# Performance work log

Measured on AMD Instinct MI355X. Metric: run time of the kernel, lower is better.

## Reference

```python
import jax, jax.numpy as jnp
import numpy as np

B, S, D = 128, 1024, 256
K = 512  # num_clusters


def setup_inputs() -> dict:
    key = jax.random.key(0)
    k1, = jax.random.split(key, 1)
    inputs = jax.random.normal(k1, (B, S, D), dtype=jnp.float32)
    # init centroids as the first K data points so no cluster is empty
    centroids = inputs.reshape(-1, D)[:K]
    return {"inputs": inputs, "centroids": centroids}


def reference(inputs, centroids):
    d = inputs.shape[-1]
    k = centroids.shape[0]
    x = inputs.reshape(-1, d)                      # [N, D]
    # squared euclidean distances via GEMM decomposition (avoids N x K x D tensor)
    x2 = jnp.sum(x * x, axis=1, keepdims=True)     # [N, 1]
    c2 = jnp.sum(centroids * centroids, axis=1)    # [K]
    dist = x2 - 2.0 * (x @ centroids.T) + c2       # [N, K]
    idx = jnp.argmin(dist, axis=-1)                # [N]
    clusters = jax.nn.one_hot(idx, k, dtype=x.dtype)   # [N, K]
    counts = jnp.sum(clusters, axis=0)             # [K]
    sums = jnp.einsum('nk,nd->kd', clusters, x)    # [K, D] scatter-reduce as GEMM
    new_centroids = sums / counts[:, None]         # [K, D]
    updated_centroids = 0.9 * centroids + 0.1 * new_centroids  # EMA update
    clusters_out = clusters.reshape(inputs.shape[:-1] + (k,))  # [B, S, K]
    return clusters_out, updated_centroids
```

## Files before the change

### kernel.cpp

```cpp
#include <hip/hip_runtime.h>
#include <hip/hip_fp16.h>

#define NPTS 131072
#define DIM  256
#define KTOT 512
#define GAP_T 0.0625f

typedef unsigned short u16;
typedef _Float16 half8 __attribute__((ext_vector_type(8)));
typedef float floatx4 __attribute__((ext_vector_type(4)));

#define WS_MAIN_NEED 8394816u

__global__ __launch_bounds__(64)
void c2_kernel(const float* __restrict__ c, double* __restrict__ c2) {
  int k = blockIdx.x;
  int lane = threadIdx.x;
  const float* row = c + (size_t)k * DIM;
  double s = 0.0;
#pragma unroll
  for (int r = 0; r < DIM / 64; ++r) {
    float v = row[r * 64 + lane];
    s += (double)v * (double)v;
  }
#pragma unroll
  for (int off = 32; off > 0; off >>= 1) s += __shfl_down(s, off);
  if (lane == 0) c2[k] = s;
}

__global__ __launch_bounds__(256)
void csplit_kernel(const float* __restrict__ c, u16* __restrict__ Ch, u16* __restrict__ Cl) {
  int id = blockIdx.x * 256 + threadIdx.x;
  int n = id >> 5;
  int cg = id & 31;
  int kc = cg >> 3, cc = cg & 7;
  const float* src = c + (size_t)n * DIM + cg * 8;
  half8 hv, lv;
#pragma unroll
  for (int e = 0; e < 8; ++e) {
    float f = src[e];
    _Float16 h = (_Float16)f;
    hv[e] = h;
    lv[e] = (_Float16)(f - (float)h);
  }
  size_t dst = (size_t)n * DIM + kc * 64 + (size_t)(cc ^ (n & 7)) * 8;
  *(half8*)(Ch + dst) = hv;
  *(half8*)(Cl + dst) = lv;
}

__device__ __forceinline__ void load_lds16(const void* g, void* l) {
  __builtin_amdgcn_global_load_lds((const __attribute__((address_space(1))) void*)g,
                                   (__attribute__((address_space(3))) void*)l, 16, 0, 0);
}

__global__ __launch_bounds__(256)
void gemm_topk_kernel(const float* __restrict__ x, const u16* __restrict__ Ch,
                      const u16* __restrict__ Cl, const double* __restrict__ c2,
                      float* __restrict__ pv1, int* __restrict__ pk1, float* __restrict__ pv2) {
  __shared__ __align__(16) unsigned char smem[128 * 132 * 4];
  __shared__ float rb_v[128], rb_v2[128];
  __shared__ int rb_k[128];
  u16* Ah = (u16*)smem;
  u16* Al = Ah + 8192;
  u16* Bh = Al + 8192;
  u16* Bl = Bh + 8192;

  const int tid = threadIdx.x;
  const int bx = blockIdx.x;
  const int nblk = bx & 3, mblk = bx >> 2;
  const int m0 = mblk * 128, n0 = nblk * 128;
  const int w = tid >> 6, lane = tid & 63;
  const int wm = (w & 1) * 64, wn = (w >> 1) * 64;
  const int lm = lane & 15, quad = lane >> 4;

  floatx4 acc[4][4] = {};

  for (int kc = 0; kc < 4; ++kc) {
    const int k0 = kc * 64;
    __syncthreads();
#pragma unroll
    for (int i = 0; i < 4; ++i) {
      int s = i * 256 + tid;
      int row = s >> 3, pos = s & 7;
      size_t go = (size_t)(n0 + row) * DIM + k0 + pos * 8;
      load_lds16(Ch + go, Bh + (size_t)s * 8);
      load_lds16(Cl + go, Bl + (size_t)s * 8);
    }
#pragma unroll
    for (int i = 0; i < 4; ++i) {
      int s = i * 256 + tid;
      int row = s >> 3, kg = s & 7;
      const float4* gx = (const float4*)(x + (size_t)(m0 + row) * DIM + k0 + kg * 8);
      float4 f0 = gx[0], f1 = gx[1];
      float fv[8] = {f0.x, f0.y, f0.z, f0.w, f1.x, f1.y, f1.z, f1.w};
      half8 hv, lv;
#pragma unroll
      for (int e = 0; e < 8; ++e) {
        _Float16 h = (_Float16)fv[e];
        hv[e] = h;
        lv[e] = (_Float16)(fv[e] - (float)h);
      }
      int pos = kg ^ (row & 7);
      *(half8*)(Ah + (size_t)row * 64 + pos * 8) = hv;
      *(half8*)(Al + (size_t)row * 64 + pos * 8) = lv;
    }
    __syncthreads();

#pragma unroll
    for (int s = 0; s < 2; ++s) {
      half8 ah[4], al[4], bh[4], bl[4];
#pragma unroll
      for (int t = 0; t < 4; ++t) {
        int m = wm + t * 16 + lm;
        int pa = ((s * 4 + quad) ^ (m & 7)) * 8;
        ah[t] = *(const half8*)(Ah + (size_t)m * 64 + pa);
        al[t] = *(const half8*)(Al + (size_t)m * 64 + pa);
        int n = wn + t * 16 + lm;
        int pb = ((s * 4 + quad) ^ (n & 7)) * 8;
        bh[t] = *(const half8*)(Bh + (size_t)n * 64 + pb);
        bl[t] = *(const half8*)(Bl + (size_t)n * 64 + pb);
      }
#pragma unroll
      for (int mt = 0; mt < 4; ++mt)
#pragma unroll
        for (int nt = 0; nt < 4; ++nt) {
          acc[mt][nt] = __builtin_amdgcn_mfma_f32_16x16x32_f16(ah[mt], bh[nt], acc[mt][nt], 0, 0, 0);
          acc[mt][nt] = __builtin_amdgcn_mfma_f32_16x16x32_f16(ah[mt], bl[nt], acc[mt][nt], 0, 0, 0);
          acc[mt][nt] = __builtin_amdgcn_mfma_f32_16x16x32_f16(al[mt], bh[nt], acc[mt][nt], 0, 0, 0);
        }
    }
  }

  __syncthreads();
  float* sc = (float*)smem;
  float c2f[4];
#pragma unroll
  for (int nt = 0; nt < 4; ++nt) c2f[nt] = (float)c2[n0 + wn + nt * 16 + lm];
#pragma unroll
  for (int mt = 0; mt < 4; ++mt)
#pragma unroll
    for (int nt = 0; nt < 4; ++nt)
#pragma unroll
      for (int r = 0; r < 4; ++r) {
        int m = wm + mt * 16 + quad * 4 + r;
        int n = wn + nt * 16 + lm;
        sc[m * 132 + n] = c2f[nt] - 2.0f * acc[mt][nt][r];
      }
  __syncthreads();

  {
    int r = tid >> 1, h = tid & 1;
    const float* rowp = sc + r * 132 + h * 64;
    float bv = 1e30f, sv = 1e30f;
    int bk = 0;
#pragma unroll 8
    for (int j = 0; j < 64; ++j) {
      float v = rowp[j];
      if (v < bv) { sv = bv; bv = v; bk = n0 + h * 64 + j; }
      else if (v < sv) sv = v;
    }
    if (h == 1) { rb_v[r] = bv; rb_k[r] = bk; rb_v2[r] = sv; }
    __syncthreads();
    if (h == 0) {
      float ov = rb_v[r], ov2 = rb_v2[r];
      int ok = rb_k[r];
      float fbv, fsv; int fbk;
      if (ov < bv) { fbv = ov; fbk = ok; fsv = fminf(bv, ov2); }
      else         { fbv = bv; fbk = bk; fsv = fminf(sv, ov); }
      int m = m0 + r;
      pv1[(size_t)nblk * NPTS + m] = fbv;
      pk1[(size_t)nblk * NPTS + m] = fbk;
      pv2[(size_t)nblk * NPTS + m] = fsv;
    }
  }
}

__global__ __launch_bounds__(256)
void combine_kernel(const float* __restrict__ pv1, const int* __restrict__ pk1,
                    const float* __restrict__ pv2, int* __restrict__ idx,
                    int* __restrict__ flagcnt, int* __restrict__ flaglist) {
  int m = blockIdx.x * 256 + threadIdx.x;
  float bv = 1e30f, sv = 1e30f;
  int bk = 0;
#pragma unroll
  for (int b = 0; b < 4; ++b) {
    float v1 = pv1[(size_t)b * NPTS + m];
    int k1 = pk1[(size_t)b * NPTS + m];
    float v2 = pv2[(size_t)b * NPTS + m];
    if (v1 < bv) { sv = fminf(bv, v2); bv = v1; bk = k1; }
    else { sv = fminf(sv, v1); }
  }
  idx[m] = bk;
  if (sv - bv < GAP_T) {
    int p = atomicAdd(flagcnt, 1);
    flaglist[p] = m;
  }
}

__global__ __launch_bounds__(256)
void refine_kernel(const float* __restrict__ x, const float* __restrict__ c,
                   const double* __restrict__ c2, const int* __restrict__ flagcnt,
                   const int* __restrict__ flaglist, int* __restrict__ idx) {
  __shared__ __align__(16) float xs[DIM];
  __shared__ double rv[256];
  __shared__ int rk[256];
  int cnt = *(volatile const int*)flagcnt;
  for (int i = blockIdx.x; i < cnt; i += gridDim.x) {
    __syncthreads();
    int m = flaglist[i];
    if (threadIdx.x < 64)
      ((float4*)xs)[threadIdx.x] = ((const float4*)(x + (size_t)m * DIM))[threadIdx.x];
    __syncthreads();
    double bestv = 1e300; int bestk = 0;
#pragma unroll
    for (int half = 0; half < 2; ++half) {
      int k = half * 256 + threadIdx.x;
      const float* crow = c + (size_t)k * DIM;
      double dacc = 0.0;
#pragma unroll
      for (int dc = 0; dc < 8; ++dc) {
        float f = 0.0f;
#pragma unroll
        for (int d = 0; d < 32; ++d) f = fmaf(xs[dc * 32 + d], crow[dc * 32 + d], f);
        dacc += (double)f;
      }
      double s = c2[k] - 2.0 * dacc;
      if (s < bestv || (s == bestv && k < bestk)) { bestv = s; bestk = k; }
    }
    rv[threadIdx.x] = bestv; rk[threadIdx.x] = bestk;
    __syncthreads();
    for (int off = 128; off > 0; off >>= 1) {
      if (threadIdx.x < off) {
        double v = rv[threadIdx.x + off]; int kk = rk[threadIdx.x + off];
        if (v < rv[threadIdx.x] || (v == rv[threadIdx.x] && kk < rk[threadIdx.x])) {
          rv[threadIdx.x] = v; rk[threadIdx.x] = kk;
        }
      }
      __syncthreads();
    }
    if (threadIdx.x == 0) idx[m] = rk[0];
  }
}

__global__ __launch_bounds__(256)
void onehot_kernel(const int* __restrict__ idx, float* __restrict__ out) {
  __shared__ int bk[32];
  int b = blockIdx.x;
  if (threadIdx.x < 32) bk[threadIdx.x] = idx[b * 32 + threadIdx.x];
  __syncthreads();
  float4* o = (float4*)(out + (size_t)b * 32 * KTOT);
#pragma unroll
  for (int j = 0; j < 16; ++j) {
    int f4 = j * 256 + threadIdx.x;
    int p = f4 >> 7;
    int n4 = (f4 & 127) * 4;
    int k = bk[p];
    float4 v;
    v.x = (k == n4 + 0) ? 1.0f : 0.0f;
    v.y = (k == n4 + 1) ? 1.0f : 0.0f;
    v.z = (k == n4 + 2) ? 1.0f : 0.0f;
    v.w = (k == n4 + 3) ? 1.0f : 0.0f;
    o[f4] = v;
  }
}

__global__ __launch_bounds__(256)
void hist_kernel(const int* __restrict__ idx, int* __restrict__ counts) {
  __shared__ int h[KTOT];
  int t = threadIdx.x;
#pragma unroll
  for (int i = 0; i < KTOT / 256; ++i) h[i * 256 + t] = 0;
  __syncthreads();
  int base = blockIdx.x * 1024 + t;
#pragma unroll
  for (int j = 0; j < 4; ++j) atomicAdd(&h[idx[base + j * 256]], 1);
  __syncthreads();
#pragma unroll
  for (int i = 0; i < KTOT / 256; ++i) {
    int v = h[i * 256 + t];
    if (v) atomicAdd(&counts[i * 256 + t], v);
  }
}

__global__ __launch_bounds__(512)
void scan_kernel(const int* __restrict__ counts, int* __restrict__ offsets,
                 int* __restrict__ cursors) {
  __shared__ int s[KTOT];
  int t = threadIdx.x;
  int mine = counts[t];
  s[t] = mine;
  __syncthreads();
  for (int off = 1; off < KTOT; off <<= 1) {
    int v = (t >= off) ? s[t - off] : 0;
    __syncthreads();
    s[t] += v;
    __syncthreads();
  }
  int excl = s[t] - mine;
  offsets[t] = excl;
  cursors[t] = excl;
  if (t == KTOT - 1) offsets[KTOT] = s[t];
}

__global__ __launch_bounds__(256)
void scatter_kernel(const int* __restrict__ idx, int* __restrict__ cursors,
                    int* __restrict__ plist) {
  int base = blockIdx.x * 1024 + threadIdx.x;
#pragma unroll
  for (int j = 0; j < 4; ++j) {
    int n = base + j * 256;
    int k = idx[n];
    int pos = atomicAdd(&cursors[k], 1);
    plist[pos] = n;
  }
}

__global__ __launch_bounds__(256)
void gathersum_flat_kernel(const float* __restrict__ x, const int* __restrict__ plist,
                           const int* __restrict__ offsets, float* __restrict__ sums) {
  __shared__ int offs[KTOT + 1];
  for (int t = threadIdx.x; t < KTOT + 1; t += 256) offs[t] = offsets[t];
  __syncthreads();
  const int w = threadIdx.x >> 6, lane = threadIdx.x & 63;
  const int wid = blockIdx.x * 4 + w;
  const int p0 = wid * 32, p1 = p0 + 32;

  int lo = 0, hi = KTOT;
  while (hi - lo > 1) { int mid = (lo + hi) >> 1; if (offs[mid] <= p0) lo = mid; else hi = mid; }
  int k = lo;

  float4 acc = make_float4(0.f, 0.f, 0.f, 0.f);
  bool any = false;
#pragma unroll 4
  for (int i = p0; i < p1; ++i) {
    while (i >= offs[k + 1]) {
      if (any) {
        float* dst = sums + (size_t)k * DIM + lane * 4;
        atomicAdd(dst + 0, acc.x); atomicAdd(dst + 1, acc.y);
        atomicAdd(dst + 2, acc.z); atomicAdd(dst + 3, acc.w);
        acc = make_float4(0.f, 0.f, 0.f, 0.f);
        any = false;
      }
      ++k;
    }
    int pid = plist[i];
    float4 v = ((const float4*)x)[(size_t)pid * 64 + lane];
    acc.x += v.x; acc.y += v.y; acc.z += v.z; acc.w += v.w;
    any = true;
  }
  if (any) {
    float* dst = sums + (size_t)k * DIM + lane * 4;
    atomicAdd(dst + 0, acc.x); atomicAdd(dst + 1, acc.y);
    atomicAdd(dst + 2, acc.z); atomicAdd(dst + 3, acc.w);
  }
}

__global__ __launch_bounds__(256)
void ema_kernel(const float* __restrict__ c, const float* __restrict__ sums,
                const int* __restrict__ counts, float* __restrict__ outc) {
  int k = blockIdx.x;
  int d = threadIdx.x;
  float cnt = (float)counts[k];
  size_t o = (size_t)k * DIM + d;
  float nc = sums[o] / cnt;
  outc[o] = 0.9f * c[o] + 0.1f * nc;
}

#define GB 4
#define SLICES 8
__global__ __launch_bounds__(256)
void sums_kernel(const float* __restrict__ x, const int* __restrict__ idx,
                 float* __restrict__ sums, int* __restrict__ counts) {
  const int groups = KTOT / GB;
  const int group = blockIdx.x % groups;
  const int slice = blockIdx.x / groups;
  const int kg0 = group * GB;
  const int tid = threadIdx.x;
  const int lane = tid & 63;
  const int w = tid >> 6;
  const int per_slice = NPTS / SLICES;
  const int nbeg = slice * per_slice;

  float4 acc[GB];
  int cnt[GB];
#pragma unroll
  for (int j = 0; j < GB; ++j) { acc[j] = make_float4(0.f, 0.f, 0.f, 0.f); cnt[j] = 0; }

  for (int it = 0; it < per_slice; it += 256) {
    int n = nbeg + it + tid;
    int k = idx[n];
#pragma unroll
    for (int j = 0; j < GB; ++j) {
      unsigned long long m = __ballot(k == kg0 + j);
      while (m) {
        int src = __ffsll((unsigned long long)m) - 1;
        int nn = __shfl(n, src);
        float4 v = ((const float4*)(x + (size_t)nn * DIM))[lane];
        acc[j].x += v.x; acc[j].y += v.y; acc[j].z += v.z; acc[j].w += v.w;
        cnt[j]++;
        m &= (m - 1);
      }
    }
  }

  __shared__ __align__(16) float lacc[4][GB][DIM];
  __shared__ int lcnt[4][GB];
#pragma unroll
  for (int j = 0; j < GB; ++j) ((float4*)&lacc[w][j][0])[lane] = acc[j];
  if (lane == 0) {
#pragma unroll
    for (int j = 0; j < GB; ++j) lcnt[w][j] = cnt[j];
  }
  __syncthreads();
#pragma unroll
  for (int j = 0; j < GB; ++j) {
    float s = lacc[0][j][tid] + lacc[1][j][tid] + lacc[2][j][tid] + lacc[3][j][tid];
    atomicAdd(&sums[(size_t)(kg0 + j) * DIM + tid], s);
  }
  if (tid < GB) {
    int ct = lcnt[0][tid] + lcnt[1][tid] + lcnt[2][tid] + lcnt[3][tid];
    atomicAdd(&counts[kg0 + tid], ct);
  }
}

#define MP 64
#define KT 64
#define DT 32
__global__ __launch_bounds__(256, 2)
void assign_kernel_r1(const float* __restrict__ x, const float* __restrict__ c,
                      const double* __restrict__ c2, float* __restrict__ out,
                      int* __restrict__ idx_out) {
  __shared__ __align__(16) float xs[DIM * MP];
  __shared__ __align__(16) float cs[DT * KT];
  const int tid = threadIdx.x;
  const int p0 = blockIdx.x * MP;
  const int tp = tid & 15;
  const int tk = tid >> 4;
  {
    const int p = tid >> 2;
    const int dg = tid & 3;
    const float4* x4 = (const float4*)(x + (size_t)(p0 + p) * DIM);
#pragma unroll
    for (int r = 0; r < 16; ++r) {
      int d4 = r * 4 + dg;
      float4 v = x4[d4];
      int dbase = d4 * 4;
      xs[(dbase + 0) * MP + p] = v.x;
      xs[(dbase + 1) * MP + p] = v.y;
      xs[(dbase + 2) * MP + p] = v.z;
      xs[(dbase + 3) * MP + p] = v.w;
    }
  }
  double best[4]; int bestk[4];
#pragma unroll
  for (int i = 0; i < 4; ++i) { best[i] = 1e300; bestk[i] = 0; }
  for (int kc = 0; kc < KTOT / KT; ++kc) {
    const int k0 = kc * KT;
    double dacc[4][4];
#pragma unroll
    for (int i = 0; i < 4; ++i)
#pragma unroll
      for (int j = 0; j < 4; ++j) dacc[i][j] = 0.0;
    for (int dc = 0; dc < DIM / DT; ++dc) {
      __syncthreads();
      {
        const int kl = tid >> 2;
        const int dg = tid & 3;
        const float4* c4 = (const float4*)(c + (size_t)(k0 + kl) * DIM + dc * DT);
#pragma unroll
        for (int h = 0; h < 2; ++h) {
          int dq = h * 4 + dg;
          float4 v = c4[dq];
          int dbase = dq * 4;
          cs[(dbase + 0) * KT + kl] = v.x;
          cs[(dbase + 1) * KT + kl] = v.y;
          cs[(dbase + 2) * KT + kl] = v.z;
          cs[(dbase + 3) * KT + kl] = v.w;
        }
      }
      __syncthreads();
      float acc[4][4];
#pragma unroll
      for (int i = 0; i < 4; ++i)
#pragma unroll
        for (int j = 0; j < 4; ++j) acc[i][j] = 0.0f;
#pragma unroll
      for (int d = 0; d < DT; ++d) {
        float4 xv = ((const float4*)(xs + (size_t)(dc * DT + d) * MP))[tp];
        float4 cv = ((const float4*)(cs + (size_t)d * KT))[tk];
        float xa[4] = {xv.x, xv.y, xv.z, xv.w};
        float ca[4] = {cv.x, cv.y, cv.z, cv.w};
#pragma unroll
        for (int i = 0; i < 4; ++i)
#pragma unroll
          for (int j = 0; j < 4; ++j) acc[i][j] = fmaf(xa[i], ca[j], acc[i][j]);
      }
#pragma unroll
      for (int i = 0; i < 4; ++i)
#pragma unroll
        for (int j = 0; j < 4; ++j) dacc[i][j] += (double)acc[i][j];
    }
#pragma unroll
    for (int j = 0; j < 4; ++j) {
      int k = k0 + tk * 4 + j;
      double c2v = c2[k];
#pragma unroll
      for (int i = 0; i < 4; ++i) {
        double s = c2v - 2.0 * dacc[i][j];
        if (s < best[i]) { best[i] = s; bestk[i] = k; }
      }
    }
  }
  __syncthreads();
  double* redv = (double*)cs;
  int* redk = (int*)xs;
  int* bk = (int*)xs + 1024;
#pragma unroll
  for (int i = 0; i < 4; ++i) {
    int p = tp * 4 + i;
    redv[tk * MP + p] = best[i];
    redk[tk * MP + p] = bestk[i];
  }
  __syncthreads();
  if (tid < MP) {
    int p = tid;
    double bv = redv[p]; int bkk = redk[p];
#pragma unroll
    for (int t = 1; t < 16; ++t) {
      double v = redv[t * MP + p]; int kk = redk[t * MP + p];
      if (v < bv || (v == bv && kk < bkk)) { bv = v; bkk = kk; }
    }
    bk[p] = bkk;
    idx_out[p0 + p] = bkk;
  }
  __syncthreads();
  float* orow = out + (size_t)p0 * KTOT;
  for (int l = tid; l < MP * KTOT; l += 256) {
    int p = l >> 9;
    int k = l & (KTOT - 1);
    orow[l] = (k == bk[p]) ? 1.0f : 0.0f;
  }
}

extern "C" void kernel_launch(void* const* d_in, const int* in_sizes, int n_in,
                              void* d_out, int out_size, void* d_ws, size_t ws_size,
                              hipStream_t stream) {
  const float* x = (const float*)d_in[0];
  const float* c = (const float*)d_in[1];
  float* out = (float*)d_out;
  float* outc = out + (size_t)NPTS * KTOT;

  char* ws = (char*)d_ws;

  if (ws_size >= WS_MAIN_NEED) {
    double* c2   = (double*)(ws + 0);
    u16* Ch      = (u16*)(ws + 4096);
    u16* Cl      = (u16*)(ws + 266240);
    int* idx     = (int*)(ws + 528384);
    float* pv1   = (float*)(ws + 1052672);
    int* pk1     = (int*)(ws + 3149824);
    float* pv2   = (float*)(ws + 5246976);
    float* sums  = (float*)(ws + 7344128);
    int* counts  = (int*)(ws + 7868416);
    int* flagcnt = (int*)(ws + 7870464);
    int* flaglist= (int*)(ws + 7870528);
    int* offsets = (int*)(ws + 1052672);
    int* cursors = (int*)(ws + 1052672 + 4096);
    int* plist   = (int*)(ws + 5246976);

    hipMemsetAsync(sums, 0, (size_t)(KTOT * DIM + KTOT) * 4, stream);
    hipMemsetAsync(flagcnt, 0, 64, stream);
    c2_kernel<<<KTOT, 64, 0, stream>>>(c, c2);
    csplit_kernel<<<64, 256, 0, stream>>>(c, Ch, Cl);
    gemm_topk_kernel<<<4096, 256, 0, stream>>>(x, Ch, Cl, c2, pv1, pk1, pv2);
    combine_kernel<<<NPTS / 256, 256, 0, stream>>>(pv1, pk1, pv2, idx, flagcnt, flaglist);
    refine_kernel<<<256, 256, 0, stream>>>(x, c, c2, flagcnt, flaglist, idx);
    onehot_kernel<<<NPTS / 32, 256, 0, stream>>>(idx, out);
    hist_kernel<<<NPTS / 1024, 256, 0, stream>>>(idx, counts);
    scan_kernel<<<1, 512, 0, stream>>>(counts, offsets, cursors);
    scatter_kernel<<<NPTS / 1024, 256, 0, stream>>>(idx, cursors, plist);
    gathersum_flat_kernel<<<NPTS / 32 / 4, 256, 0, stream>>>(x, plist, offsets, sums);
    ema_kernel<<<KTOT, DIM, 0, stream>>>(c, sums, counts, outc);
  } else {
    double* c2  = (double*)ws;
    int* idx    = (int*)(ws + 4096);
    float* sums = (float*)(ws + 4096 + 524288);
    int* counts = (int*)(ws + 4096 + 524288 + 524288);
    hipMemsetAsync(sums, 0, (size_t)(KTOT * DIM + KTOT) * 4, stream);
    c2_kernel<<<KTOT, 64, 0, stream>>>(c, c2);
    assign_kernel_r1<<<NPTS / MP, 256, 0, stream>>>(x, c, c2, out, idx);
    sums_kernel<<<(KTOT / GB) * SLICES, 256, 0, stream>>>(x, idx, sums, counts);
    ema_kernel<<<KTOT, DIM, 0, stream>>>(c, sums, counts, outc);
  }
}
```

Measured before the change: 730.4 us.

## Batch refinement of ambiguous points into tiled GEMM and tighten gap threshold

The per-point refine kernel is replaced by a batched kernel that processes 64 flagged points per block with shared-memory tiles of x and centroids, so centroid loads are reused across points instead of re-read for each one. The gap threshold that decides which points need exact fp32/fp64 refinement is lowered, so far fewer points get flagged. The top-2 scan in the GEMM epilogue now reads shared memory as float4. A smaller threshold risks missing points whose half-precision-split distances are ambiguous beyond the new margin, which could change the argmin result.

```diff
diff --git a/kernel.cpp b/kernel.cpp
--- a/kernel.cpp
+++ b/kernel.cpp
@@ -4,7 +4,7 @@
 #define NPTS 131072
 #define DIM  256
 #define KTOT 512
-#define GAP_T 0.0625f
+#define GAP_T 0.012f
 
 typedef unsigned short u16;
 typedef _Float16 half8 __attribute__((ext_vector_type(8)));
@@ -150,14 +150,19 @@
 
   {
     int r = tid >> 1, h = tid & 1;
-    const float* rowp = sc + r * 132 + h * 64;
+    const float4* rowp4 = (const float4*)(sc + r * 132 + h * 64);
     float bv = 1e30f, sv = 1e30f;
     int bk = 0;
-#pragma unroll 8
-    for (int j = 0; j < 64; ++j) {
-      float v = rowp[j];
-      if (v < bv) { sv = bv; bv = v; bk = n0 + h * 64 + j; }
-      else if (v < sv) sv = v;
+#pragma unroll
+    for (int j4 = 0; j4 < 16; ++j4) {
+      float4 v4 = rowp4[j4];
+      float va[4] = {v4.x, v4.y, v4.z, v4.w};
+#pragma unroll
+      for (int e = 0; e < 4; ++e) {
+        float v = va[e];
+        if (v < bv) { sv = bv; bv = v; bk = n0 + h * 64 + j4 * 4 + e; }
+        else if (v < sv) sv = v;
+      }
     }
     if (h == 1) { rb_v[r] = bv; rb_k[r] = bk; rb_v2[r] = sv; }
     __syncthreads();
@@ -197,48 +202,129 @@
   }
 }
 
-__global__ __launch_bounds__(256)
-void refine_kernel(const float* __restrict__ x, const float* __restrict__ c,
-                   const double* __restrict__ c2, const int* __restrict__ flagcnt,
-                   const int* __restrict__ flaglist, int* __restrict__ idx) {
-  __shared__ __align__(16) float xs[DIM];
-  __shared__ double rv[256];
-  __shared__ int rk[256];
+#define MP 64
+#define KT 64
+#define DT 32
+__global__ __launch_bounds__(256, 2)
+void refine_batch_kernel(const float* __restrict__ x, const float* __restrict__ c,
+                         const double* __restrict__ c2, const int* __restrict__ flagcnt,
+                         const int* __restrict__ flaglist, int* __restrict__ idx) {
+  __shared__ __align__(16) float xs[DIM * MP];
+  __shared__ __align__(16) float cs[DT * KT];
+  __shared__ int plds[MP];
+  const int tid = threadIdx.x;
   int cnt = *(volatile const int*)flagcnt;
-  for (int i = blockIdx.x; i < cnt; i += gridDim.x) {
-    __syncthreads();
-    int m = flaglist[i];
-    if (threadIdx.x < 64)
-      ((float4*)xs)[threadIdx.x] = ((const float4*)(x + (size_t)m * DIM))[threadIdx.x];
-    __syncthreads();
-    double bestv = 1e300; int bestk = 0;
-#pragma unroll
-    for (int half = 0; half < 2; ++half) {
-      int k = half * 256 + threadIdx.x;
-      const float* crow = c + (size_t)k * DIM;
-      double dacc = 0.0;
-#pragma unroll
-      for (int dc = 0; dc < 8; ++dc) {
-        float f = 0.0f;
-#pragma unroll
-        for (int d = 0; d < 32; ++d) f = fmaf(xs[dc * 32 + d], crow[dc * 32 + d], f);
-        dacc += (double)f;
-      }
-      double s = c2[k] - 2.0 * dacc;
-      if (s < bestv || (s == bestv && k < bestk)) { bestv = s; bestk = k; }
-    }
-    rv[threadIdx.x] = bestv; rk[threadIdx.x] = bestk;
-    __syncthreads();
-    for (int off = 128; off > 0; off >>= 1) {
-      if (threadIdx.x < off) {
-        double v = rv[threadIdx.x + off]; int kk = rk[threadIdx.x + off];
-        if (v < rv[threadIdx.x] || (v == rv[threadIdx.x] && kk < rk[threadIdx.x])) {
-          rv[threadIdx.x] = v; rk[threadIdx.x] = kk;
+  int nbatch = (cnt + MP - 1) / MP;
+
+  for (int b = blockIdx.x; b < nbatch; b += gridDim.x) {
+    __syncthreads();
+    int base = b * MP;
+    if (tid < MP) {
+      int i = base + tid;
+      plds[tid] = (i < cnt) ? flaglist[i] : flaglist[base];
+    }
+    __syncthreads();
+
+    {
+      const int p = tid >> 2;
+      const int dg = tid & 3;
+      const float4* x4 = (const float4*)(x + (size_t)plds[p] * DIM);
+#pragma unroll
+      for (int r = 0; r < 16; ++r) {
+        int d4 = r * 4 + dg;
+        float4 v = x4[d4];
+        int dbase = d4 * 4;
+        xs[(dbase + 0) * MP + p] = v.x;
+        xs[(dbase + 1) * MP + p] = v.y;
+        xs[(dbase + 2) * MP + p] = v.z;
+        xs[(dbase + 3) * MP + p] = v.w;
+      }
+    }
+
+    const int tp = tid & 15;
+    const int tk = tid >> 4;
+    double best[4]; int bestk[4];
+#pragma unroll
+    for (int i = 0; i < 4; ++i) { best[i] = 1e300; bestk[i] = 0; }
+
+    for (int kc = 0; kc < KTOT / KT; ++kc) {
+      const int k0 = kc * KT;
+      double dacc[4][4];
+#pragma unroll
+      for (int i = 0; i < 4; ++i)
+#pragma unroll
+        for (int j = 0; j < 4; ++j) dacc[i][j] = 0.0;
+      for (int dc = 0; dc < DIM / DT; ++dc) {
+        __syncthreads();
+        {
+          const int kl = tid >> 2;
+          const int dg = tid & 3;
+          const float4* c4 = (const float4*)(c + (size_t)(k0 + kl) * DIM + dc * DT);
+#pragma unroll
+          for (int h = 0; h < 2; ++h) {
+            int dq = h * 4 + dg;
+            float4 v = c4[dq];
+            int dbase = dq * 4;
+            cs[(dbase + 0) * KT + kl] = v.x;
+            cs[(dbase + 1) * KT + kl] = v.y;
+            cs[(dbase + 2) * KT + kl] = v.z;
+            cs[(dbase + 3) * KT + kl] = v.w;
+          }
         }
-      }
-      __syncthreads();
-    }
-    if (threadIdx.x == 0) idx[m] = rk[0];
+        __syncthreads();
+        float acc[4][4];
+#pragma unroll
+        for (int i = 0; i < 4; ++i)
+#pragma unroll
+          for (int j = 0; j < 4; ++j) acc[i][j] = 0.0f;
+#pragma unroll
+        for (int d = 0; d < DT; ++d) {
+          float4 xv = ((const float4*)(xs + (size_t)(dc * DT + d) * MP))[tp];
+          float4 cv = ((const float4*)(cs + (size_t)d * KT))[tk];
+          float xa[4] = {xv.x, xv.y, xv.z, xv.w};
+          float ca[4] = {cv.x, cv.y, cv.z, cv.w};
+#pragma unroll
+          for (int i = 0; i < 4; ++i)
+#pragma unroll
+            for (int j = 0; j < 4; ++j) acc[i][j] = fmaf(xa[i], ca[j], acc[i][j]);
+        }
+#pragma unroll
+        for (int i = 0; i < 4; ++i)
+#pragma unroll
+          for (int j = 0; j < 4; ++j) dacc[i][j] += (double)acc[i][j];
+      }
+#pragma unroll
+      for (int j = 0; j < 4; ++j) {
+        int k = k0 + tk * 4 + j;
+        double c2v = c2[k];
+#pragma unroll
+        for (int i = 0; i < 4; ++i) {
+          double s = c2v - 2.0 * dacc[i][j];
+          if (s < best[i]) { best[i] = s; bestk[i] = k; }
+        }
+      }
+    }
+
+    __syncthreads();
+    double* redv = (double*)cs;
+    int* redk = (int*)xs;
+#pragma unroll
+    for (int i = 0; i < 4; ++i) {
+      int p = tp * 4 + i;
+      redv[tk * MP + p] = best[i];
+      redk[tk * MP + p] = bestk[i];
+    }
+    __syncthreads();
+    if (tid < MP) {
+      int p = tid;
+      double bv = redv[p]; int bkk = redk[p];
+#pragma unroll
+      for (int t = 1; t < 16; ++t) {
+        double v = redv[t * MP + p]; int kk = redk[t * MP + p];
+        if (v < bv || (v == bv && kk < bkk)) { bv = v; bkk = kk; }
+      }
+      if (base + p < cnt) idx[plds[p]] = bkk;
+    }
   }
 }
 
@@ -423,9 +509,6 @@
   }
 }
 
-#define MP 64
-#define KT 64
-#define DT 32
 __global__ __launch_bounds__(256, 2)
 void assign_kernel_r1(const float* __restrict__ x, const float* __restrict__ c,
                       const double* __restrict__ c2, float* __restrict__ out,
@@ -574,7 +657,7 @@
     csplit_kernel<<<64, 256, 0, stream>>>(c, Ch, Cl);
     gemm_topk_kernel<<<4096, 256, 0, stream>>>(x, Ch, Cl, c2, pv1, pk1, pv2);
     combine_kernel<<<NPTS / 256, 256, 0, stream>>>(pv1, pk1, pv2, idx, flagcnt, flaglist);
-    refine_kernel<<<256, 256, 0, stream>>>(x, c, c2, flagcnt, flaglist, idx);
+    refine_batch_kernel<<<256, 256, 0, stream>>>(x, c, c2, flagcnt, flaglist, idx);
     onehot_kernel<<<NPTS / 32, 256, 0, stream>>>(idx, out);
     hist_kernel<<<NPTS / 1024, 256, 0, stream>>>(idx, counts);
     scan_kernel<<<1, 512, 0, stream>>>(counts, offsets, cursors);
```

Result: slower. 886.0 us (+21.3%).
